# Optimization experiments

Measured on AMD Instinct MI355X. Metric: run time of the kernel, lower is better.

The kernel has to match this reference:

```python
import jax, jax.numpy as jnp
import numpy as np

N_HEAD = 16
TEMPERATURE = 1.0
LORA_SCALING = 16.0 / 8.0  # lora_alpha / r


def setup_inputs() -> dict:
    key = jax.random.key(0)
    B, S, D, E, R = 4, 1024, 1024, 8, 8
    ks = jax.random.split(key, 24)
    it = iter(ks)

    def nrm(shape, s):
        return (jax.random.normal(next(it), shape, jnp.float32) * s)

    inp = {}
    inp['x'] = jax.random.normal(next(it), (B, S, D), jnp.float32)
    inp['conv_w'] = nrm((D, D, 3), 0.02)
    inp['conv_b'] = jnp.zeros((D,), jnp.float32)
    inp['pool_w'] = nrm((1, D), 0.02)
    inp['pool_b'] = jnp.zeros((1,), jnp.float32)
    inp['rlin_w'] = nrm((E, D), 0.02)
    inp['rlin_b'] = jnp.zeros((E,), jnp.float32)
    for p, has_bias in (('q', True), ('k', False), ('v', True), ('o', True)):
        inp[p + 'W'] = nrm((D, D), 0.02)
        if has_bias:
            inp[p + 'b'] = jnp.zeros((D,), jnp.float32)
        inp[p + 'A'] = nrm((E, R, D), 0.02)
        inp[p + 'B'] = nrm((E, D, R), 0.02)
    return inp


def _router(x, conv_w, conv_b, pool_w, pool_b, rlin_w, rlin_b):
    # Conv1d(kernel=3, padding=1) over sequence, channels = n_state
    xc = jax.lax.conv_general_dilated(
        x.transpose(0, 2, 1), conv_w, (1,), [(1, 1)],
        dimension_numbers=('NCH', 'OIH', 'NCH')) + conv_b[None, :, None]
    xp = xc.transpose(0, 2, 1)                      # [B, S, D]
    scores = xp @ pool_w.T + pool_b                 # [B, S, 1]
    w = jax.nn.softmax(scores, axis=1)
    pooled = jnp.sum(w * xp, axis=1)                # [B, D]
    logits = pooled @ rlin_w.T + rlin_b             # [B, E]
    return jax.nn.softmax(logits / TEMPERATURE, axis=-1)


def _moe_linear(x, W, b, A, Bm, route):
    base = x @ W.T
    if b is not None:
        base = base + b
    h = jnp.einsum('bsd,erd->besr', x, A)           # [B, E, S, r]
    lora = jnp.einsum('besr,enr,be->bsn', h, Bm, route)
    return base + LORA_SCALING * lora


def reference(x, conv_w, conv_b, pool_w, pool_b, rlin_w, rlin_b,
              qW, qb, qA, qB, kW, kA, kB, vW, vb, vA, vB, oW, ob, oA, oB):
    B, S, D = x.shape
    H = N_HEAD
    dh = D // H
    route = _router(x, conv_w, conv_b, pool_w, pool_b, rlin_w, rlin_b)

    q = _moe_linear(x, qW, qb, qA, qB, route)
    k = _moe_linear(x, kW, None, kA, kB, route)
    v = _moe_linear(x, vW, vb, vA, vB, route)

    scale = dh ** (-0.25)
    qh = q.reshape(B, S, H, dh).transpose(0, 2, 1, 3) * scale   # [B,H,S,dh]
    kh = k.reshape(B, S, H, dh).transpose(0, 2, 3, 1) * scale   # [B,H,dh,S]
    vh = v.reshape(B, S, H, dh).transpose(0, 2, 1, 3)           # [B,H,S,dh]

    qk = (qh @ kh).astype(jnp.float32)                          # [B,H,S,S]
    w = jax.nn.softmax(qk, axis=-1).astype(q.dtype)
    wv = (w @ vh).transpose(0, 2, 1, 3).reshape(B, S, D)

    out = _moe_linear(wv, oW, ob, oA, oB, route)
    return out, qk
```

## Files before the change

### kernel.cpp

```cpp
#include <hip/hip_runtime.h>
#include <cstdint>

typedef unsigned short u16;
typedef __bf16 bf16_t;
typedef bf16_t bf16x8 __attribute__((ext_vector_type(8)));
typedef float f32x4 __attribute__((ext_vector_type(4)));

#define B_ 4
#define S_ 1024
#define D_ 1024
#define E_ 8
#define R_ 8
#define H_ 16
#define DH_ 64

#define GLOAD16(gp, lp) __builtin_amdgcn_global_load_lds( \
        (const __attribute__((address_space(1))) void*)(gp), \
        (__attribute__((address_space(3))) void*)(lp), 16, 0, 0)

static __device__ __forceinline__ u16 f2b(float f){
    union { float f; uint32_t i; } v; v.f = f;
    uint32_t i = v.i;
    uint32_t r = i + 0x7FFFu + ((i >> 16) & 1u);
    return (u16)(r >> 16);
}

__global__ void k_cvt4(const float4* src, ushort4* dst, int n4){
    for (int i = blockIdx.x*blockDim.x + threadIdx.x; i < n4; i += gridDim.x*blockDim.x){
        float4 v = src[i];
        ushort4 o;
        o.x = f2b(v.x); o.y = f2b(v.y); o.z = f2b(v.z); o.w = f2b(v.w);
        dst[i] = o;
    }
}

__global__ void k_cvtB(const float* qB, const float* kB, const float* vB, const float* oB,
                       u16* dst, float* cwp){
    const float* src = (blockIdx.y==0)?qB:(blockIdx.y==1)?kB:(blockIdx.y==2)?vB:oB;
    u16* d = dst + (size_t)blockIdx.y*E_*D_*R_;
    for (int i = blockIdx.x*blockDim.x + threadIdx.x; i < E_*D_*R_; i += gridDim.x*blockDim.x)
        d[i] = f2b(src[i]);
    if (blockIdx.x == 0 && blockIdx.y == 0)
        for (int i = threadIdx.x; i < 3*D_; i += blockDim.x) cwp[i] = 0.f;
}

__global__ void k_cwp(const float* conv_w, const float* conv_b, const float* pool_w,
                      const float* pool_b, float* cwp, float* constk){
    __shared__ float red[256];
    int bid = blockIdx.x, ob = blockIdx.y;
    if (bid < 12){
        int j = bid*256 + threadIdx.x;
        int t = j >> 10, i = j & 1023;
        float acc = 0.f;
        for (int o = ob*128; o < (ob+1)*128; ++o)
            acc += pool_w[o] * conv_w[(size_t)o*3072 + i*3 + t];
        atomicAdd(&cwp[j], acc);
    } else if (ob == 0){
        float acc = 0.f;
        for (int o = threadIdx.x; o < D_; o += 256) acc += pool_w[o] * conv_b[o];
        red[threadIdx.x] = acc; __syncthreads();
        for (int s = 128; s > 0; s >>= 1){
            if (threadIdx.x < s) red[threadIdx.x] += red[threadIdx.x+s];
            __syncthreads();
        }
        if (threadIdx.x == 0) *constk = red[0] + pool_b[0];
    }
}

__global__ void k_h(const float* x, const float* cwp, float* h){
    int b = blockIdx.y;
    int w = threadIdx.x >> 6, lane = threadIdx.x & 63;
    int s = blockIdx.x*4 + w;
    const float4* xr = (const float4*)(x + ((size_t)b*S_ + s)*D_);
    const float4* c0 = (const float4*)(cwp);
    const float4* c1 = (const float4*)(cwp + D_);
    const float4* c2 = (const float4*)(cwp + 2*D_);
    float a0 = 0.f, a1 = 0.f, a2 = 0.f;
    #pragma unroll
    for (int it = 0; it < 4; ++it){
        float4 v  = xr[it*64 + lane];
        float4 w0 = c0[it*64 + lane];
        float4 w1 = c1[it*64 + lane];
        float4 w2 = c2[it*64 + lane];
        a0 += v.x*w0.x + v.y*w0.y + v.z*w0.z + v.w*w0.w;
        a1 += v.x*w1.x + v.y*w1.y + v.z*w1.z + v.w*w1.w;
        a2 += v.x*w2.x + v.y*w2.y + v.z*w2.z + v.w*w2.w;
    }
    for (int off = 32; off; off >>= 1){
        a0 += __shfl_down(a0, off);
        a1 += __shfl_down(a1, off);
        a2 += __shfl_down(a2, off);
    }
    if (lane == 0){
        h[(0*B_ + b)*S_ + s] = a0;
        h[(1*B_ + b)*S_ + s] = a1;
        h[(2*B_ + b)*S_ + s] = a2;
    }
}

__global__ void k_softw(const float* h, const float* constk, float* wsm){
    int b = blockIdx.x;
    const float* h0 = h + (0*B_ + b)*S_;
    const float* h1 = h + (1*B_ + b)*S_;
    const float* h2 = h + (2*B_ + b)*S_;
    float ck = *constk;
    __shared__ float red[256];
    float mx = -1e30f;
    for (int s = threadIdx.x; s < S_; s += 256){
        float v = h1[s] + ck;
        if (s >= 1)     v += h0[s-1];
        if (s+1 < S_)   v += h2[s+1];
        mx = fmaxf(mx, v);
    }
    red[threadIdx.x] = mx; __syncthreads();
    for (int st = 128; st > 0; st >>= 1){
        if (threadIdx.x < st) red[threadIdx.x] = fmaxf(red[threadIdx.x], red[threadIdx.x+st]);
        __syncthreads();
    }
    mx = red[0]; __syncthreads();
    float sum = 0.f;
    for (int s = threadIdx.x; s < S_; s += 256){
        float v = h1[s] + ck;
        if (s >= 1)     v += h0[s-1];
        if (s+1 < S_)   v += h2[s+1];
        sum += __expf(v - mx);
    }
    red[threadIdx.x] = sum; __syncthreads();
    for (int st = 128; st > 0; st >>= 1){
        if (threadIdx.x < st) red[threadIdx.x] += red[threadIdx.x+st];
        __syncthreads();
    }
    float inv = 1.f / red[0];
    for (int s = threadIdx.x; s < S_; s += 256){
        float v = h1[s] + ck;
        if (s >= 1)     v += h0[s-1];
        if (s+1 < S_)   v += h2[s+1];
        wsm[b*S_+s] = __expf(v - mx) * inv;
    }
}

__global__ void k_xw(const float* x, const float* wsm, float* xwl){
    int b = blockIdx.y;
    int lane = threadIdx.x & 63;
    int w = threadIdx.x >> 6;
    int i = blockIdx.x*64 + lane;
    const float* xb = x + (size_t)b*S_*D_;
    float a0 = 0.f, a1 = 0.f, a2 = 0.f;
    #pragma unroll 4
    for (int r = w*256; r < (w+1)*256; ++r){
        float xv = xb[(size_t)r*D_ + i];
        float w1 = wsm[b*S_ + r];
        float w0 = (r+1 < S_) ? wsm[b*S_ + r + 1] : 0.f;
        float w2 = (r >= 1)   ? wsm[b*S_ + r - 1] : 0.f;
        a0 += w0*xv; a1 += w1*xv; a2 += w2*xv;
    }
    __shared__ float red[3][4][64];
    red[0][w][lane] = a0; red[1][w][lane] = a1; red[2][w][lane] = a2;
    __syncthreads();
    if (w == 0){
        a0 = red[0][0][lane] + red[0][1][lane] + red[0][2][lane] + red[0][3][lane];
        a1 = red[1][0][lane] + red[1][1][lane] + red[1][2][lane] + red[1][3][lane];
        a2 = red[2][0][lane] + red[2][1][lane] + red[2][2][lane] + red[2][3][lane];
        xwl[b*3072 + i*3 + 0] = a0;
        xwl[b*3072 + i*3 + 1] = a1;
        xwl[b*3072 + i*3 + 2] = a2;
    }
}

__global__ void k_pooled(const float* conv_w, const float* conv_b, const float* xwl, float* pooled){
    int o = blockIdx.x*4 + (threadIdx.x >> 6);
    int lane = threadIdx.x & 63;
    const float* cw = conv_w + (size_t)o*3072;
    float a0=0.f, a1=0.f, a2=0.f, a3=0.f;
    for (int j = lane; j < 3072; j += 64){
        float c = cw[j];
        a0 += c*xwl[j]; a1 += c*xwl[3072+j]; a2 += c*xwl[2*3072+j]; a3 += c*xwl[3*3072+j];
    }
    for (int off = 32; off; off >>= 1){
        a0 += __shfl_down(a0, off); a1 += __shfl_down(a1, off);
        a2 += __shfl_down(a2, off); a3 += __shfl_down(a3, off);
    }
    if (lane == 0){
        float cb = conv_b[o];
        pooled[0*D_+o] = a0+cb; pooled[1*D_+o] = a1+cb;
        pooled[2*D_+o] = a2+cb; pooled[3*D_+o] = a3+cb;
    }
}

__global__ void k_route(const float* pooled, const float* rlin_w, const float* rlin_b, float* route){
    __shared__ float lg[B_][E_];
    int t = threadIdx.x;
    int b = t >> 6, e = (t >> 3) & 7, part = t & 7;
    float acc = 0.f;
    for (int o = part; o < D_; o += 8) acc += pooled[b*D_+o] * rlin_w[e*D_+o];
    acc += __shfl_down(acc, 4); acc += __shfl_down(acc, 2); acc += __shfl_down(acc, 1);
    if (part == 0) lg[b][e] = acc + rlin_b[e];
    __syncthreads();
    if (t < B_){
        float mx = -1e30f;
        for (int e2 = 0; e2 < E_; ++e2) mx = fmaxf(mx, lg[t][e2]);
        float ex[E_], sum = 0.f;
        for (int e2 = 0; e2 < E_; ++e2){ ex[e2] = expf(lg[t][e2]-mx); sum += ex[e2]; }
        for (int e2 = 0; e2 < E_; ++e2) route[t*E_+e2] = ex[e2]/sum;
    }
}

__global__ void k_aeff(const float* qA, const float* kA, const float* vA, const float* oA,
                       const float* route, u16* AeffT){
    int dc = blockIdx.x, b = blockIdx.y, p = blockIdx.z;
    const float* Ap = (p==0)?qA:(p==1)?kA:(p==2)?vA:oA;
    int z = p*4 + b;
    for (int idx = threadIdx.x; idx < 64*64; idx += 256){
        int dl = idx >> 6, kk = idx & 63;
        int d = dc*64 + dl;
        int e = kk >> 3, r = kk & 7;
        float v = 2.0f * route[b*E_+e] * Ap[(size_t)(e*R_+r)*D_ + d];
        AeffT[((size_t)z*D_ + d)*64 + kk] = f2b(v);
    }
}

__global__ __launch_bounds__(256) void k_weff(
        const u16* B16,
        const float* qW, const float* kW, const float* vW, const float* oW,
        const u16* AeffT, u16* Weff){
    __shared__ __align__(16) u16 As[128*64];
    __shared__ __align__(16) u16 Bs[128*64];
    int z = blockIdx.z, p = z >> 2;
    const u16* Bp = B16 + (size_t)p*E_*D_*R_;
    const float* Wp = (p==0)?qW:(p==1)?kW:(p==2)?vW:oW;
    int n0 = blockIdx.x*128, d0 = blockIdx.y*128;
    int tid = threadIdx.x;
    int e = tid & 7, row = tid >> 3;
    for (int pass = 0; pass < 4; ++pass){
        int rr = row + pass*32;
        GLOAD16(&Bp[((size_t)e*D_ + (n0+rr))*R_],           &As[pass*2048 + tid*8]);
        GLOAD16(&AeffT[((size_t)z*D_ + (d0+rr))*64 + e*8],  &Bs[pass*2048 + tid*8]);
    }
    __syncthreads();
    int l = tid & 63, w = tid >> 6;
    int wm = (w & 1)*64, wn = (w >> 1)*64;
    int lr = l & 15, quad = l >> 4;
    f32x4 acc[4][4] = {};
    for (int kk = 0; kk < 64; kk += 32){
        bf16x8 af[4], bg[4];
        for (int i = 0; i < 4; ++i) af[i] = *(const bf16x8*)&As[(wm + i*16 + lr)*64 + kk + quad*8];
        for (int j = 0; j < 4; ++j) bg[j] = *(const bf16x8*)&Bs[(wn + j*16 + lr)*64 + kk + quad*8];
        for (int i = 0; i < 4; ++i)
            for (int j = 0; j < 4; ++j)
                acc[i][j] = __builtin_amdgcn_mfma_f32_16x16x32_bf16(af[i], bg[j], acc[i][j], 0, 0, 0);
    }
    u16* Wz = Weff + (size_t)z*D_*D_;
    for (int i = 0; i < 4; ++i)
        for (int j = 0; j < 4; ++j)
            for (int r2 = 0; r2 < 4; ++r2){
                int n = n0 + wm + i*16 + quad*4 + r2;
                int d = d0 + wn + j*16 + lr;
                Wz[(size_t)n*D_ + d] = f2b(acc[i][j][r2] + Wp[(size_t)n*D_ + d]);
            }
}

static __device__ __forceinline__ void gemm_body(
        const u16* __restrict__ A, int lda,
        const u16* __restrict__ Bw,
        u16* Cb, float* Cf, int ldc,
        const float* bias, float scale, int K,
        int m0, int n0)
{
    __shared__ __align__(16) u16 As[128*32];
    __shared__ __align__(16) u16 Bs[128*32];
    int tid = threadIdx.x;
    int srow = tid >> 2, skc = (tid & 3)*8;
    u16* asd = &As[tid*8];
    u16* bsd = &Bs[tid*8];
    const u16* ga0 = &A [(size_t)(m0+srow)*lda + skc];
    const u16* ga1 = &A [(size_t)(m0+srow+64)*lda + skc];
    const u16* gb0 = &Bw[(size_t)(n0+srow)*D_ + skc];
    const u16* gb1 = &Bw[(size_t)(n0+srow+64)*D_ + skc];
    int l = tid & 63, w = tid >> 6;
    int wm = (w & 1)*64, wn = (w >> 1)*64;
    int lr = l & 15, quad = l >> 4;
    f32x4 acc[4][4] = {};
    for (int k0 = 0; k0 < K; k0 += 32){
        __syncthreads();
        GLOAD16(ga0 + k0, asd);
        GLOAD16(ga1 + k0, asd + 2048);
        GLOAD16(gb0 + k0, bsd);
        GLOAD16(gb1 + k0, bsd + 2048);
        __syncthreads();
        bf16x8 af[4], bg[4];
        for (int i = 0; i < 4; ++i) af[i] = *(const bf16x8*)&As[(wm + i*16 + lr)*32 + quad*8];
        for (int j = 0; j < 4; ++j) bg[j] = *(const bf16x8*)&Bs[(wn + j*16 + lr)*32 + quad*8];
        for (int i = 0; i < 4; ++i)
            for (int j = 0; j < 4; ++j)
                acc[i][j] = __builtin_amdgcn_mfma_f32_16x16x32_bf16(af[i], bg[j], acc[i][j], 0, 0, 0);
    }
    for (int j = 0; j < 4; ++j){
        int n = n0 + wn + j*16 + lr;
        float bv = bias ? bias[n] : 0.f;
        for (int i = 0; i < 4; ++i){
            int mrow = m0 + wm + i*16 + quad*4;
            for (int r2 = 0; r2 < 4; ++r2){
                float val = (acc[i][j][r2] + bv) * scale;
                size_t idx = (size_t)(mrow+r2)*ldc + n;
                if (Cf) __builtin_nontemporal_store(val, &Cf[idx]);
                else    Cb[idx] = f2b(val);
            }
        }
    }
}

__global__ __launch_bounds__(256) void k_gemm_qkv(
        const u16* x16, const u16* Weff, u16* qkv, const float* qb, const float* vb){
    int z = blockIdx.z, p = z >> 2, b = z & 3;
    const float* bias = (p==0) ? qb : (p==2) ? vb : (const float*)nullptr;
    float scale = (p==2) ? 1.0f : 0.35355339059327373f;
    gemm_body(x16 + (size_t)b*S_*D_, D_,
              Weff + (size_t)z*D_*D_,
              qkv + (size_t)z*S_*D_, (float*)nullptr, D_,
              bias, scale, 1024, blockIdx.x*128, blockIdx.y*128);
}

__global__ __launch_bounds__(256) void k_gemm_o(
        const u16* wv, const u16* WeffO, float* out, const float* ob){
    int b = blockIdx.z;
    gemm_body(wv + (size_t)b*S_*D_, D_,
              WeffO + (size_t)b*D_*D_,
              (u16*)nullptr, out + (size_t)b*S_*D_, D_,
              ob, 1.0f, 1024, blockIdx.x*128, blockIdx.y*128);
}

__global__ void k_vtrans(const u16* v, u16* vT){
    __shared__ __align__(16) u16 Tl[64*72];
    int st = blockIdx.x, bh = blockIdx.y;
    int b = bh >> 4, h = bh & 15;
    int tid = threadIdx.x;
    int row = tid >> 3, c = (tid & 7)*8;
    const u16* vb = v + (size_t)b*S_*D_ + h*64;
    for (int pass = 0; pass < 2; ++pass){
        int r = row + pass*32;
        *(uint4*)&Tl[r*72 + c] = *(const uint4*)&vb[(size_t)(st*64 + r)*D_ + c];
    }
    __syncthreads();
    u16* vTb = vT + (size_t)bh*64*S_;
    for (int pass = 0; pass < 2; ++pass){
        int dr = row + pass*32;
        union { u16 s[8]; uint4 u; } tmp;
        for (int j = 0; j < 8; ++j) tmp.s[j] = Tl[(c+j)*72 + dr];
        *(uint4*)&vTb[(size_t)dr*S_ + st*64 + c] = tmp.u;
    }
}

__global__ __launch_bounds__(256) void k_attn(const u16* q, const u16* k, const u16* vT,
                                              float* qk_out, u16* wv){
    __shared__ __align__(16) u16 Ql[64*72];
    __shared__ __align__(16) u16 Kl[64*72];
    __shared__ __align__(16) u16 Vt[64*72];
    __shared__ __align__(16) u16 Pl[64*72];
    int qt = blockIdx.x, bh = blockIdx.y;
    int b = bh >> 4, h = bh & 15;
    int q0 = qt*64;
    int tid = threadIdx.x;
    int row = tid >> 3, c = (tid & 7)*8;
    int l = tid & 63, w = tid >> 6;
    int lr = l & 15, quad = l >> 4;
    const u16* qp  = q  + (size_t)b*S_*D_ + h*64;
    const u16* kp  = k  + (size_t)b*S_*D_ + h*64;
    const u16* vTp = vT + (size_t)bh*64*S_;
    float* qko = qk_out + (size_t)bh*S_*S_;
    for (int pass = 0; pass < 2; ++pass){
        int r = row + pass*32;
        *(uint4*)&Ql[r*72 + c] = *(const uint4*)&qp[(size_t)(q0 + r)*D_ + c];
    }
    f32x4 oacc[4] = {};
    float m_i[4], l_i[4];
    for (int r2 = 0; r2 < 4; ++r2){ m_i[r2] = -1e30f; l_i[r2] = 0.f; }
    for (int t0 = 0; t0 < S_; t0 += 64){
        __syncthreads();
        for (int pass = 0; pass < 2; ++pass){
            int r = row + pass*32;
            *(uint4*)&Kl[r*72 + c] = *(const uint4*)&kp[(size_t)(t0 + r)*D_ + c];
            *(uint4*)&Vt[r*72 + c] = *(const uint4*)&vTp[(size_t)r*S_ + t0 + c];
        }
        __syncthreads();
        f32x4 sacc[4] = {};
        for (int kk = 0; kk < 64; kk += 32){
            bf16x8 aq = *(const bf16x8*)&Ql[(w*16 + lr)*72 + kk + quad*8];
            for (int jn = 0; jn < 4; ++jn){
                bf16x8 bk = *(const bf16x8*)&Kl[(jn*16 + lr)*72 + kk + quad*8];
                sacc[jn] = __builtin_amdgcn_mfma_f32_16x16x32_bf16(aq, bk, sacc[jn], 0, 0, 0);
            }
        }
        for (int jn = 0; jn < 4; ++jn)
            for (int r2 = 0; r2 < 4; ++r2){
                int sq = q0 + w*16 + quad*4 + r2;
                __builtin_nontemporal_store(sacc[jn][r2], &qko[(size_t)sq*S_ + t0 + jn*16 + lr]);
            }
        float alpha[4];
        for (int r2 = 0; r2 < 4; ++r2){
            float mx = fmaxf(fmaxf(sacc[0][r2], sacc[1][r2]), fmaxf(sacc[2][r2], sacc[3][r2]));
            for (int off = 1; off < 16; off <<= 1) mx = fmaxf(mx, __shfl_xor(mx, off));
            float mnew = fmaxf(m_i[r2], mx);
            alpha[r2] = __expf(m_i[r2] - mnew);
            m_i[r2] = mnew;
        }
        f32x4 p[4];
        for (int jn = 0; jn < 4; ++jn)
            for (int r2 = 0; r2 < 4; ++r2)
                p[jn][r2] = __expf(sacc[jn][r2] - m_i[r2]);
        for (int r2 = 0; r2 < 4; ++r2){
            float s = p[0][r2] + p[1][r2] + p[2][r2] + p[3][r2];
            for (int off = 1; off < 16; off <<= 1) s += __shfl_xor(s, off);
            l_i[r2] = l_i[r2]*alpha[r2] + s;
        }
        for (int jn = 0; jn < 4; ++jn)
            for (int r2 = 0; r2 < 4; ++r2)
                oacc[jn][r2] *= alpha[r2];
        for (int jn = 0; jn < 4; ++jn)
            for (int r2 = 0; r2 < 4; ++r2)
                Pl[(w*16 + quad*4 + r2)*72 + jn*16 + lr] = f2b(p[jn][r2]);
        for (int kk = 0; kk < 64; kk += 32){
            bf16x8 ap = *(const bf16x8*)&Pl[(w*16 + lr)*72 + kk + quad*8];
            for (int jn = 0; jn < 4; ++jn){
                bf16x8 bv = *(const bf16x8*)&Vt[(jn*16 + lr)*72 + kk + quad*8];
                oacc[jn] = __builtin_amdgcn_mfma_f32_16x16x32_bf16(ap, bv, oacc[jn], 0, 0, 0);
            }
        }
    }
    u16* wvp = wv + (size_t)b*S_*D_ + h*64;
    for (int r2 = 0; r2 < 4; ++r2){
        float inv = 1.f / l_i[r2];
        int sq = q0 + w*16 + quad*4 + r2;
        for (int jn = 0; jn < 4; ++jn)
            wvp[(size_t)sq*D_ + jn*16 + lr] = f2b(oacc[jn][r2] * inv);
    }
}

extern "C" void kernel_launch(void* const* d_in, const int* in_sizes, int n_in,
                              void* d_out, int out_size, void* d_ws, size_t ws_size,
                              hipStream_t stream){
    const float* x      = (const float*)d_in[0];
    const float* conv_w = (const float*)d_in[1];
    const float* conv_b = (const float*)d_in[2];
    const float* pool_w = (const float*)d_in[3];
    const float* pool_b = (const float*)d_in[4];
    const float* rlin_w = (const float*)d_in[5];
    const float* rlin_b = (const float*)d_in[6];
    const float* qW = (const float*)d_in[7];
    const float* qb = (const float*)d_in[8];
    const float* qA = (const float*)d_in[9];
    const float* qB = (const float*)d_in[10];
    const float* kW = (const float*)d_in[11];
    const float* kA = (const float*)d_in[12];
    const float* kB = (const float*)d_in[13];
    const float* vW = (const float*)d_in[14];
    const float* vb = (const float*)d_in[15];
    const float* vA = (const float*)d_in[16];
    const float* vB = (const float*)d_in[17];
    const float* oW = (const float*)d_in[18];
    const float* ob = (const float*)d_in[19];
    const float* oA = (const float*)d_in[20];
    const float* oB = (const float*)d_in[21];

    char* ws = (char*)d_ws;
    float* route  = (float*)(ws + 0);
    float* constk = (float*)(ws + 512);
    float* cwp    = (float*)(ws + 1024);
    float* h      = (float*)(ws + 16384);
    float* wsm    = (float*)(ws + 65536);
    float* xwl    = (float*)(ws + 81920);
    float* pooled = (float*)(ws + 131072);
    u16* AeffT = (u16*)(ws + (1ull  << 20));
    u16* B16   = (u16*)(ws + (3ull  << 20));
    u16* Weff  = (u16*)(ws + (4ull  << 20));
    u16* x16   = (u16*)(ws + (36ull << 20));
    u16* qkv   = (u16*)(ws + (44ull << 20));
    u16* qbuf  = qkv + 0*(size_t)B_*S_*D_;
    u16* kbuf  = qkv + 1*(size_t)B_*S_*D_;
    u16* vbuf  = qkv + 2*(size_t)B_*S_*D_;
    u16* vTbuf = (u16*)(ws + (68ull << 20));
    u16* wvbuf = vbuf;

    float* out    = (float*)d_out;
    float* qk_out = out + (size_t)B_*S_*D_;

    const long long sDD = (long long)D_*D_;

    k_cvt4<<<2048, 256, 0, stream>>>((const float4*)x, (ushort4*)x16, B_*S_*D_/4);
    k_cvtB<<<dim3(16, 4), 256, 0, stream>>>(qB, kB, vB, oB, B16, cwp);

    k_cwp   <<<dim3(13, 8), 256, 0, stream>>>(conv_w, conv_b, pool_w, pool_b, cwp, constk);
    k_h     <<<dim3(S_/4, B_), 256, 0, stream>>>(x, cwp, h);
    k_softw <<<B_, 256, 0, stream>>>(h, constk, wsm);
    k_xw    <<<dim3(16, B_), 256, 0, stream>>>(x, wsm, xwl);
    k_pooled<<<256, 256, 0, stream>>>(conv_w, conv_b, xwl, pooled);
    k_route <<<1, 256, 0, stream>>>(pooled, rlin_w, rlin_b, route);
    k_aeff  <<<dim3(16, B_, 4), 256, 0, stream>>>(qA, kA, vA, oA, route, AeffT);
    k_weff  <<<dim3(8, 8, 16), 256, 0, stream>>>(B16, qW, kW, vW, oW, AeffT, Weff);

    k_gemm_qkv<<<dim3(8,8,12), 256, 0, stream>>>(x16, Weff, qkv, qb, vb);

    k_vtrans<<<dim3(16, B_*H_), 256, 0, stream>>>(vbuf, vTbuf);
    k_attn  <<<dim3(16, B_*H_), 256, 0, stream>>>(qbuf, kbuf, vTbuf, qk_out, wvbuf);
    k_gemm_o<<<dim3(8,8,B_), 256, 0, stream>>>(wvbuf, Weff + 12*sDD, out, ob);
}
```

Before: 684.7 us.

## Fuse conversion and softmax kernels, use swizzled async LDS loads in attention

Merges the x and LoRA-B bf16 conversion kernels into one launch, and folds the per-batch sequence softmax into the x-weighted-sum kernel so it is recomputed per block in shared memory instead of going through a separate launch and global buffer. The attention kernel drops padded LDS rows in favour of an XOR-swizzled layout and stages Q/K/V tiles with global_load_lds direct-to-LDS loads. Together these cut launch overhead and register traffic for staging, at the cost of redundant softmax work per block and more complex index math.

```diff
diff --git a/kernel.cpp b/kernel.cpp
--- a/kernel.cpp
+++ b/kernel.cpp
@@ -25,23 +25,30 @@
     return (u16)(r >> 16);
 }
 
-__global__ void k_cvt4(const float4* src, ushort4* dst, int n4){
-    for (int i = blockIdx.x*blockDim.x + threadIdx.x; i < n4; i += gridDim.x*blockDim.x){
-        float4 v = src[i];
-        ushort4 o;
-        o.x = f2b(v.x); o.y = f2b(v.y); o.z = f2b(v.z); o.w = f2b(v.w);
-        dst[i] = o;
-    }
-}
-
-__global__ void k_cvtB(const float* qB, const float* kB, const float* vB, const float* oB,
-                       u16* dst, float* cwp){
-    const float* src = (blockIdx.y==0)?qB:(blockIdx.y==1)?kB:(blockIdx.y==2)?vB:oB;
-    u16* d = dst + (size_t)blockIdx.y*E_*D_*R_;
-    for (int i = blockIdx.x*blockDim.x + threadIdx.x; i < E_*D_*R_; i += gridDim.x*blockDim.x)
-        d[i] = f2b(src[i]);
-    if (blockIdx.x == 0 && blockIdx.y == 0)
-        for (int i = threadIdx.x; i < 3*D_; i += blockDim.x) cwp[i] = 0.f;
+__global__ void k_cvtall(const float4* x, const float* qB, const float* kB,
+                         const float* vB, const float* oB,
+                         ushort4* x16, ushort4* B16v, float4* cwp4){
+    const int NX = B_*S_*D_/4;
+    const int NB = E_*D_*R_/4;
+    const int NC = 3*D_/4;
+    const int NTOT = NX + 4*NB + NC;
+    for (int i = blockIdx.x*blockDim.x + threadIdx.x; i < NTOT; i += gridDim.x*blockDim.x){
+        if (i < NX){
+            float4 v = x[i];
+            ushort4 o; o.x=f2b(v.x); o.y=f2b(v.y); o.z=f2b(v.z); o.w=f2b(v.w);
+            x16[i] = o;
+        } else if (i < NX + 4*NB){
+            int j = i - NX;
+            int p = j >> 14, e = j & (NB-1);
+            const float4* src = (p==0)?(const float4*)qB:(p==1)?(const float4*)kB
+                              :(p==2)?(const float4*)vB:(const float4*)oB;
+            float4 v = src[e];
+            ushort4 o; o.x=f2b(v.x); o.y=f2b(v.y); o.z=f2b(v.z); o.w=f2b(v.w);
+            B16v[p*NB + e] = o;
+        } else {
+            cwp4[i - NX - 4*NB] = make_float4(0.f,0.f,0.f,0.f);
+        }
+    }
 }
 
 __global__ void k_cwp(const float* conv_w, const float* conv_b, const float* pool_w,
@@ -98,18 +105,24 @@
     }
 }
 
-__global__ void k_softw(const float* h, const float* constk, float* wsm){
-    int b = blockIdx.x;
+__global__ void k_xw(const float* x, const float* h, const float* constk, float* xwl){
+    int b = blockIdx.y;
+    int lane = threadIdx.x & 63;
+    int w = threadIdx.x >> 6;
+    int i = blockIdx.x*64 + lane;
+    __shared__ float red[256];
+    __shared__ float wsm_l[S_];
+    __shared__ float red3[3][4][64];
     const float* h0 = h + (0*B_ + b)*S_;
     const float* h1 = h + (1*B_ + b)*S_;
     const float* h2 = h + (2*B_ + b)*S_;
     float ck = *constk;
-    __shared__ float red[256];
     float mx = -1e30f;
     for (int s = threadIdx.x; s < S_; s += 256){
         float v = h1[s] + ck;
-        if (s >= 1)     v += h0[s-1];
-        if (s+1 < S_)   v += h2[s+1];
+        if (s >= 1)   v += h0[s-1];
+        if (s+1 < S_) v += h2[s+1];
+        wsm_l[s] = v;
         mx = fmaxf(mx, v);
     }
     red[threadIdx.x] = mx; __syncthreads();
@@ -119,48 +132,33 @@
     }
     mx = red[0]; __syncthreads();
     float sum = 0.f;
-    for (int s = threadIdx.x; s < S_; s += 256){
-        float v = h1[s] + ck;
-        if (s >= 1)     v += h0[s-1];
-        if (s+1 < S_)   v += h2[s+1];
-        sum += __expf(v - mx);
-    }
+    for (int s = threadIdx.x; s < S_; s += 256) sum += __expf(wsm_l[s] - mx);
     red[threadIdx.x] = sum; __syncthreads();
     for (int st = 128; st > 0; st >>= 1){
         if (threadIdx.x < st) red[threadIdx.x] += red[threadIdx.x+st];
         __syncthreads();
     }
     float inv = 1.f / red[0];
-    for (int s = threadIdx.x; s < S_; s += 256){
-        float v = h1[s] + ck;
-        if (s >= 1)     v += h0[s-1];
-        if (s+1 < S_)   v += h2[s+1];
-        wsm[b*S_+s] = __expf(v - mx) * inv;
-    }
-}
-
-__global__ void k_xw(const float* x, const float* wsm, float* xwl){
-    int b = blockIdx.y;
-    int lane = threadIdx.x & 63;
-    int w = threadIdx.x >> 6;
-    int i = blockIdx.x*64 + lane;
+    __syncthreads();
+    for (int s = threadIdx.x; s < S_; s += 256)
+        wsm_l[s] = __expf(wsm_l[s] - mx) * inv;
+    __syncthreads();
     const float* xb = x + (size_t)b*S_*D_;
     float a0 = 0.f, a1 = 0.f, a2 = 0.f;
     #pragma unroll 4
     for (int r = w*256; r < (w+1)*256; ++r){
         float xv = xb[(size_t)r*D_ + i];
-        float w1 = wsm[b*S_ + r];
-        float w0 = (r+1 < S_) ? wsm[b*S_ + r + 1] : 0.f;
-        float w2 = (r >= 1)   ? wsm[b*S_ + r - 1] : 0.f;
+        float w1 = wsm_l[r];
+        float w0 = (r+1 < S_) ? wsm_l[r+1] : 0.f;
+        float w2 = (r >= 1)   ? wsm_l[r-1] : 0.f;
         a0 += w0*xv; a1 += w1*xv; a2 += w2*xv;
     }
-    __shared__ float red[3][4][64];
-    red[0][w][lane] = a0; red[1][w][lane] = a1; red[2][w][lane] = a2;
+    red3[0][w][lane] = a0; red3[1][w][lane] = a1; red3[2][w][lane] = a2;
     __syncthreads();
     if (w == 0){
-        a0 = red[0][0][lane] + red[0][1][lane] + red[0][2][lane] + red[0][3][lane];
-        a1 = red[1][0][lane] + red[1][1][lane] + red[1][2][lane] + red[1][3][lane];
-        a2 = red[2][0][lane] + red[2][1][lane] + red[2][2][lane] + red[2][3][lane];
+        a0 = red3[0][0][lane] + red3[0][1][lane] + red3[0][2][lane] + red3[0][3][lane];
+        a1 = red3[1][0][lane] + red3[1][1][lane] + red3[1][2][lane] + red3[1][3][lane];
+        a2 = red3[2][0][lane] + red3[2][1][lane] + red3[2][2][lane] + red3[2][3][lane];
         xwl[b*3072 + i*3 + 0] = a0;
         xwl[b*3072 + i*3 + 1] = a1;
         xwl[b*3072 + i*3 + 2] = a2;
@@ -352,41 +350,42 @@
 
 __global__ __launch_bounds__(256) void k_attn(const u16* q, const u16* k, const u16* vT,
                                               float* qk_out, u16* wv){
-    __shared__ __align__(16) u16 Ql[64*72];
-    __shared__ __align__(16) u16 Kl[64*72];
-    __shared__ __align__(16) u16 Vt[64*72];
-    __shared__ __align__(16) u16 Pl[64*72];
+    __shared__ __align__(16) u16 Ql[64*64];
+    __shared__ __align__(16) u16 Kl[64*64];
+    __shared__ __align__(16) u16 Vt[64*64];
+    __shared__ __align__(16) u16 Pl[64*64];
     int qt = blockIdx.x, bh = blockIdx.y;
     int b = bh >> 4, h = bh & 15;
     int q0 = qt*64;
     int tid = threadIdx.x;
-    int row = tid >> 3, c = (tid & 7)*8;
     int l = tid & 63, w = tid >> 6;
     int lr = l & 15, quad = l >> 4;
+    int srow = tid >> 3;
+    int scol = (((tid & 7) ^ ((tid >> 3) & 7))) * 8;
+    int sdst = tid * 8;
     const u16* qp  = q  + (size_t)b*S_*D_ + h*64;
     const u16* kp  = k  + (size_t)b*S_*D_ + h*64;
     const u16* vTp = vT + (size_t)bh*64*S_;
     float* qko = qk_out + (size_t)bh*S_*S_;
-    for (int pass = 0; pass < 2; ++pass){
-        int r = row + pass*32;
-        *(uint4*)&Ql[r*72 + c] = *(const uint4*)&qp[(size_t)(q0 + r)*D_ + c];
-    }
+    GLOAD16(&qp[(size_t)(q0 + srow)*D_ + scol],      &Ql[sdst]);
+    GLOAD16(&qp[(size_t)(q0 + srow + 32)*D_ + scol], &Ql[sdst + 2048]);
+    int rsw = lr & 7;
     f32x4 oacc[4] = {};
     float m_i[4], l_i[4];
     for (int r2 = 0; r2 < 4; ++r2){ m_i[r2] = -1e30f; l_i[r2] = 0.f; }
     for (int t0 = 0; t0 < S_; t0 += 64){
         __syncthreads();
-        for (int pass = 0; pass < 2; ++pass){
-            int r = row + pass*32;
-            *(uint4*)&Kl[r*72 + c] = *(const uint4*)&kp[(size_t)(t0 + r)*D_ + c];
-            *(uint4*)&Vt[r*72 + c] = *(const uint4*)&vTp[(size_t)r*S_ + t0 + c];
-        }
+        GLOAD16(&kp[(size_t)(t0 + srow)*D_ + scol],        &Kl[sdst]);
+        GLOAD16(&kp[(size_t)(t0 + srow + 32)*D_ + scol],   &Kl[sdst + 2048]);
+        GLOAD16(&vTp[(size_t)srow*S_ + t0 + scol],         &Vt[sdst]);
+        GLOAD16(&vTp[(size_t)(srow + 32)*S_ + t0 + scol],  &Vt[sdst + 2048]);
         __syncthreads();
         f32x4 sacc[4] = {};
         for (int kk = 0; kk < 64; kk += 32){
-            bf16x8 aq = *(const bf16x8*)&Ql[(w*16 + lr)*72 + kk + quad*8];
+            int un = ((quad + (kk >> 3)) ^ rsw) * 8;
+            bf16x8 aq = *(const bf16x8*)&Ql[(w*16 + lr)*64 + un];
             for (int jn = 0; jn < 4; ++jn){
-                bf16x8 bk = *(const bf16x8*)&Kl[(jn*16 + lr)*72 + kk + quad*8];
+                bf16x8 bk = *(const bf16x8*)&Kl[(jn*16 + lr)*64 + un];
                 sacc[jn] = __builtin_amdgcn_mfma_f32_16x16x32_bf16(aq, bk, sacc[jn], 0, 0, 0);
             }
         }
@@ -416,12 +415,16 @@
             for (int r2 = 0; r2 < 4; ++r2)
                 oacc[jn][r2] *= alpha[r2];
         for (int jn = 0; jn < 4; ++jn)
-            for (int r2 = 0; r2 < 4; ++r2)
-                Pl[(w*16 + quad*4 + r2)*72 + jn*16 + lr] = f2b(p[jn][r2]);
+            for (int r2 = 0; r2 < 4; ++r2){
+                int pr = w*16 + quad*4 + r2;
+                int tu = (jn*2 + (lr >> 3)) ^ (pr & 7);
+                Pl[pr*64 + tu*8 + (lr & 7)] = f2b(p[jn][r2]);
+            }
         for (int kk = 0; kk < 64; kk += 32){
-            bf16x8 ap = *(const bf16x8*)&Pl[(w*16 + lr)*72 + kk + quad*8];
+            int un = ((quad + (kk >> 3)) ^ rsw) * 8;
+            bf16x8 ap = *(const bf16x8*)&Pl[(w*16 + lr)*64 + un];
             for (int jn = 0; jn < 4; ++jn){
-                bf16x8 bv = *(const bf16x8*)&Vt[(jn*16 + lr)*72 + kk + quad*8];
+                bf16x8 bv = *(const bf16x8*)&Vt[(jn*16 + lr)*64 + un];
                 oacc[jn] = __builtin_amdgcn_mfma_f32_16x16x32_bf16(ap, bv, oacc[jn], 0, 0, 0);
             }
         }
@@ -466,7 +469,6 @@
     float* constk = (float*)(ws + 512);
     float* cwp    = (float*)(ws + 1024);
     float* h      = (float*)(ws + 16384);
-    float* wsm    = (float*)(ws + 65536);
     float* xwl    = (float*)(ws + 81920);
     float* pooled = (float*)(ws + 131072);
     u16* AeffT = (u16*)(ws + (1ull  << 20));
@@ -485,13 +487,12 @@
 
     const long long sDD = (long long)D_*D_;
 
-    k_cvt4<<<2048, 256, 0, stream>>>((const float4*)x, (ushort4*)x16, B_*S_*D_/4);
-    k_cvtB<<<dim3(16, 4), 256, 0, stream>>>(qB, kB, vB, oB, B16, cwp);
+    k_cvtall<<<2048, 256, 0, stream>>>((const float4*)x, qB, kB, vB, oB,
+                                       (ushort4*)x16, (ushort4*)B16, (float4*)cwp);
 
     k_cwp   <<<dim3(13, 8), 256, 0, stream>>>(conv_w, conv_b, pool_w, pool_b, cwp, constk);
     k_h     <<<dim3(S_/4, B_), 256, 0, stream>>>(x, cwp, h);
-    k_softw <<<B_, 256, 0, stream>>>(h, constk, wsm);
-    k_xw    <<<dim3(16, B_), 256, 0, stream>>>(x, wsm, xwl);
+    k_xw    <<<dim3(16, B_), 256, 0, stream>>>(x, h, constk, xwl);
     k_pooled<<<256, 256, 0, stream>>>(conv_w, conv_b, xwl, pooled);
     k_route <<<1, 256, 0, stream>>>(pooled, rlin_w, rlin_b, route);
     k_aeff  <<<dim3(16, B_, 4), 256, 0, stream>>>(qA, kA, vA, oA, route, AeffT);
```

After: 615.1 us. 1.11x faster.
